# Performance work log

Measured on AMD Instinct MI355X. Metric: run time of the kernel, lower is better.

The kernel has to match this reference:

```python
import jax, jax.numpy as jnp
import numpy as np

NUM_EMBEDDINGS = 1024
EMBEDDING_DIM = 256
COMMITMENT_COST = 0.25


def setup_inputs() -> dict:
    key = jax.random.key(0)
    k1, k2 = jax.random.split(key)
    z = jax.random.normal(k1, (64, 32, 32, EMBEDDING_DIM), dtype=jnp.float32)
    # torch init: uniform(-1/num_embeddings, 1/num_embeddings)
    codebook = jax.random.uniform(
        k2, (NUM_EMBEDDINGS, EMBEDDING_DIM), dtype=jnp.float32,
        minval=-1.0 / NUM_EMBEDDINGS, maxval=1.0 / NUM_EMBEDDINGS)
    return {"z": z, "codebook": codebook}


def reference(z, codebook):
    sg = jax.lax.stop_gradient
    D = codebook.shape[1]
    flat_z = z.reshape(-1, D)  # [N, D]
    # squared L2 distances: ||z||^2 + ||e||^2 - 2 z.e  -> [N, K]
    distances = (jnp.sum(flat_z * flat_z, axis=1, keepdims=True)
                 + jnp.sum(codebook * codebook, axis=1)
                 - 2.0 * jnp.matmul(flat_z, codebook.T))
    indices = jnp.argmin(distances, axis=1)  # [N]
    quantized = codebook[indices].reshape(z.shape)
    e_latent_loss = jnp.mean((quantized - sg(z)) ** 2)
    q_latent_loss = jnp.mean((z - sg(quantized)) ** 2)
    vq_loss = e_latent_loss + COMMITMENT_COST * q_latent_loss
    # straight-through estimator
    quantized_st = z + sg(quantized - z)
    return quantized_st, vq_loss, indices.reshape(z.shape[:-1])
```

## Files before the change

kernel.cpp:

```cpp
#include <hip/hip_runtime.h>

#pragma clang fp contract(off)


#define NROWS   65536
#define DDIM    256
#define KCODES  1024
#define QSIZE   (NROWS * DDIM)
#define LOSS_OFF QSIZE
#define IDX_OFF (QSIZE + 1)
#define MARGIN  3.0e-4f
#define RCAP    16384
#define RBATCH  16

typedef __bf16 bf16x8 __attribute__((ext_vector_type(8)));
typedef float f32x4 __attribute__((ext_vector_type(4)));
typedef unsigned int u32;
typedef unsigned long long u64;
typedef unsigned short u16;

#define GLOAD_LDS16(gsrc, ldst) \
    __builtin_amdgcn_global_load_lds( \
        (const __attribute__((address_space(1))) u32*)(gsrc), \
        (__attribute__((address_space(3))) u32*)(ldst), 16, 0, 0)

__device__ __forceinline__ u32 omap(float s) {
    u32 u = __float_as_uint(s);
    return (u & 0x80000000u) ? ~u : (u | 0x80000000u);
}
__device__ __forceinline__ u64 pack_key(float s, u32 j) {
    return ((u64)omap(s) << 32) | j;
}

__device__ __forceinline__ float pw128_sq(const float* __restrict__ x) {
    float r[8];
    #pragma unroll
    for (int j = 0; j < 8; ++j) r[j] = x[j] * x[j];
    for (int i = 8; i < 128; i += 8)
        #pragma unroll
        for (int j = 0; j < 8; ++j) r[j] += x[i + j] * x[i + j];
    return ((r[0] + r[1]) + (r[2] + r[3])) + ((r[4] + r[5]) + (r[6] + r[7]));
}

__global__ __launch_bounds__(256) void vq_pack_cb(
    const float* __restrict__ E, u16* __restrict__ ebh,
    float4* __restrict__ etp,
    float* __restrict__ ee, float* __restrict__ sum, int* __restrict__ count) {
    int j = blockIdx.x * 256 + threadIdx.x;
    if (j == 0) { *sum = 0.0f; *count = 0; }
    if (j >= KCODES) return;
    const float* row = E + (size_t)j * DDIM;
    const float4* row4 = (const float4*)row;
    #pragma unroll
    for (int d4 = 0; d4 < DDIM / 4; ++d4) etp[d4 * KCODES + j] = row4[d4];
    #pragma unroll
    for (int ks = 0; ks < 32; ++ks) {
        bf16x8 h8;
        #pragma unroll
        for (int e = 0; e < 8; ++e) h8[e] = (__bf16)row[ks * 8 + e];
        *(bf16x8*)(ebh + ((size_t)ks * KCODES + j) * 8) = h8;
    }
    ee[j] = pw128_sq(row) + pw128_sq(row + 128);
}

__device__ __forceinline__ void stage_chunk32(
    const u16* __restrict__ ebh, int codebase, char* buf, int t) {
    #pragma unroll
    for (int i = 0; i < 4; ++i) {
        int p = t + 256 * i;
        int ks = p >> 5, c = p & 31;
        GLOAD_LDS16(ebh + ((size_t)ks * KCODES + codebase + c) * 8, buf + p * 16);
    }
}

__global__ __launch_bounds__(256, 4) void vq_gemm(
    const float* __restrict__ Z,
    const u16* __restrict__ ebh,
    const float* __restrict__ ee,
    float* __restrict__ s1c, float* __restrict__ s2c, float* __restrict__ i1c,
    float* __restrict__ sum) {
    __shared__ __align__(16) char bs[3][16384];
    const int t = threadIdx.x, w = t >> 6, l = t & 63;
    const int lr = l & 15, lg = l >> 4;
    const int rowtile = blockIdx.x >> 1, half = blockIdx.x & 1;
    const int rowbase = rowtile * 128;
    const int codebase = half * 512;

    bf16x8 aH[2][8];
    float ss = 0.0f;
    #pragma unroll
    for (int rf = 0; rf < 2; ++rf) {
        const float* zr = Z + (size_t)(rowbase + w * 32 + rf * 16 + lr) * DDIM;
        #pragma unroll
        for (int s = 0; s < 8; ++s) {
            const float4* src = (const float4*)(zr + (s * 4 + lg) * 8);
            float4 v0 = src[0], v1 = src[1];
            bf16x8 h8;
            h8[0] = (__bf16)v0.x; h8[1] = (__bf16)v0.y;
            h8[2] = (__bf16)v0.z; h8[3] = (__bf16)v0.w;
            h8[4] = (__bf16)v1.x; h8[5] = (__bf16)v1.y;
            h8[6] = (__bf16)v1.z; h8[7] = (__bf16)v1.w;
            aH[rf][s] = h8;
            ss += v0.x * v0.x + v0.y * v0.y + v0.z * v0.z + v0.w * v0.w
                + v1.x * v1.x + v1.y * v1.y + v1.z * v1.z + v1.w * v1.w;
        }
    }
    if (half == 0) {
        #pragma unroll
        for (int off = 1; off < 64; off <<= 1) ss += __shfl_xor(ss, off);
        if (l == 0) atomicAdd(sum, ss);
    }

    float s1[2][4], s2[2][4]; int i1[2][4];
    #pragma unroll
    for (int rf = 0; rf < 2; ++rf)
        #pragma unroll
        for (int r = 0; r < 4; ++r) { s1[rf][r] = 1e30f; s2[rf][r] = 1e30f; i1[rf][r] = 0x7FFFFFFF; }

    stage_chunk32(ebh, codebase, bs[0], t);
    stage_chunk32(ebh, codebase + 32, bs[1], t);
    for (int ch = 0; ch < 16; ++ch) {
        if (ch < 15) { asm volatile("s_waitcnt vmcnt(4)" ::: "memory"); }
        else         { asm volatile("s_waitcnt vmcnt(0)" ::: "memory"); }
        __builtin_amdgcn_sched_barrier(0);
        __builtin_amdgcn_s_barrier();
        if (ch + 2 < 16) stage_chunk32(ebh, codebase + (ch + 2) * 32, bs[(ch + 2) % 3], t);
        const char* buf = bs[ch % 3];
        const int chbase = codebase + ch * 32;

        f32x4 acc[2][2];
        #pragma unroll
        for (int rf = 0; rf < 2; ++rf)
            #pragma unroll
            for (int cf = 0; cf < 2; ++cf) acc[rf][cf] = 0.0f;

        #pragma unroll
        for (int s = 0; s < 8; ++s) {
            #pragma unroll
            for (int cf = 0; cf < 2; ++cf) {
                int off = (((s * 4 + lg) * 32 + cf * 16 + lr) * 16);
                bf16x8 bh = *(const bf16x8*)(buf + off);
                #pragma unroll
                for (int rf = 0; rf < 2; ++rf)
                    acc[rf][cf] = __builtin_amdgcn_mfma_f32_16x16x32_bf16(aH[rf][s], bh, acc[rf][cf], 0, 0, 0);
            }
        }
        #pragma unroll
        for (int cf = 0; cf < 2; ++cf) {
            int code = chbase + cf * 16 + lr;
            float e2c = ee[code];
            #pragma unroll
            for (int rf = 0; rf < 2; ++rf)
                #pragma unroll
                for (int r = 0; r < 4; ++r) {
                    float v = __fmaf_rn(-2.0f, acc[rf][cf][r], e2c);
                    float so = s1[rf][r];
                    s2[rf][r] = fminf(fmaxf(so, v), s2[rf][r]);
                    bool lt = v < so;
                    s1[rf][r] = lt ? v : so;
                    i1[rf][r] = lt ? code : i1[rf][r];
                }
        }
    }
    #pragma unroll
    for (int off = 1; off < 16; off <<= 1) {
        #pragma unroll
        for (int rf = 0; rf < 2; ++rf)
            #pragma unroll
            for (int r = 0; r < 4; ++r) {
                float os1 = __shfl_xor(s1[rf][r], off);
                float os2 = __shfl_xor(s2[rf][r], off);
                int   oi  = __shfl_xor(i1[rf][r], off);
                float ns2 = fminf(fmaxf(s1[rf][r], os1), fminf(s2[rf][r], os2));
                bool take = (os1 < s1[rf][r]) || (os1 == s1[rf][r] && oi < i1[rf][r]);
                s1[rf][r] = take ? os1 : s1[rf][r];
                i1[rf][r] = take ? oi : i1[rf][r];
                s2[rf][r] = ns2;
            }
    }
    if (lr == 0) {
        #pragma unroll
        for (int rf = 0; rf < 2; ++rf)
            #pragma unroll
            for (int r = 0; r < 4; ++r) {
                size_t idx = (size_t)half * NROWS + rowbase + w * 32 + rf * 16 + lg * 4 + r;
                s1c[idx] = s1[rf][r];
                s2c[idx] = s2[rf][r];
                i1c[idx] = (float)i1[rf][r];
            }
    }
}

__global__ __launch_bounds__(256) void vq_combine(
    const float* __restrict__ s1c, const float* __restrict__ s2c,
    const float* __restrict__ i1c,
    float* out, float* __restrict__ sum, int* __restrict__ count,
    int* __restrict__ list) {
    const int r = blockIdx.x * 256 + threadIdx.x;
    float s1a = s1c[r], s1b = s1c[NROWS + r];
    float s2a = s2c[r], s2b = s2c[NROWS + r];
    int   ia  = (int)i1c[r], ib = (int)i1c[NROWS + r];
    bool tb = s1b < s1a;
    float s1 = tb ? s1b : s1a;
    int   i1 = tb ? ib : ia;
    float s2 = tb ? fminf(s2b, s1a) : fminf(s2a, s1b);
    out[(size_t)IDX_OFF + r] = (float)i1;
    if (s2 <= s1 + MARGIN) {
        int slot = atomicAdd(count, 1);
        if (slot < RCAP) list[slot] = r;
    }
    #pragma unroll
    for (int off = 1; off < 64; off <<= 1) s1 += __shfl_xor(s1, off);
    if ((threadIdx.x & 63) == 0) atomicAdd(sum, s1);
}

__global__ __launch_bounds__(256) void vq_rescue(
    const float* __restrict__ Z, const float4* __restrict__ etp,
    const float* __restrict__ ee, const int* __restrict__ count,
    const int* __restrict__ list, const float* __restrict__ sum, float* out) {
    __shared__ float zrow[RBATCH][DDIM];
    __shared__ float zacc[RBATCH][16];
    __shared__ float z2s[RBATCH];
    __shared__ u64 rmin[RBATCH];
    __shared__ int rowid[RBATCH];
    const int t = threadIdx.x;
    if (blockIdx.x == 0 && t == 0) out[LOSS_OFF] = 1.25f * (*sum) / (float)QSIZE;
    int n = *count; if (n > RCAP) n = RCAP;
    const int base = blockIdx.x * RBATCH;
    if (base >= n) return;
    int nb = n - base; if (nb > RBATCH) nb = RBATCH;

    if (t < RBATCH) {
        rowid[t] = (t < nb) ? list[base + t] : 0;
        rmin[t] = ~0ULL;
    }
    __syncthreads();
    #pragma unroll
    for (int i = 0; i < RBATCH * (DDIM / 4) / 256; ++i) {
        int p = t + 256 * i;
        int r = p >> 6, c4 = p & 63;
        if (r < nb) ((float4*)zrow[r])[c4] =
            ((const float4*)(Z + (size_t)rowid[r] * DDIM))[c4];
    }
    __syncthreads();
    if (t < RBATCH * 8) {
        int r = t >> 3, j = t & 7;
        const float* zr = zrow[r];
        float a0 = zr[j] * zr[j], a1 = zr[128 + j] * zr[128 + j];
        for (int i = 8; i < 128; i += 8) {
            a0 += zr[i + j] * zr[i + j];
            a1 += zr[128 + i + j] * zr[128 + i + j];
        }
        zacc[r][j] = a0; zacc[r][8 + j] = a1;
    }
    __syncthreads();
    if (t < RBATCH) {
        const float* a = zacc[t];
        float c0 = ((a[0] + a[1]) + (a[2] + a[3])) + ((a[4] + a[5]) + (a[6] + a[7]));
        float c1 = ((a[8] + a[9]) + (a[10] + a[11])) + ((a[12] + a[13]) + (a[14] + a[15]));
        z2s[t] = c0 + c1;
    }
    __syncthreads();

    float acc[4][RBATCH];
    #pragma unroll
    for (int c = 0; c < 4; ++c)
        #pragma unroll
        for (int r = 0; r < RBATCH; ++r) acc[c][r] = 0.0f;

    for (int d4 = 0; d4 < DDIM / 4; ++d4) {
        float4 ev[4];
        #pragma unroll
        for (int c = 0; c < 4; ++c)
            ev[c] = etp[(size_t)d4 * KCODES + t + c * 256];
        #pragma unroll
        for (int r = 0; r < RBATCH; ++r) {
            float4 zv = ((const float4*)zrow[r])[d4];
            #pragma unroll
            for (int c = 0; c < 4; ++c) {
                float a = acc[c][r];
                a = __fmaf_rn(zv.x, ev[c].x, a); a = __fmaf_rn(zv.y, ev[c].y, a);
                a = __fmaf_rn(zv.z, ev[c].z, a); a = __fmaf_rn(zv.w, ev[c].w, a);
                acc[c][r] = a;
            }
        }
    }
    float e2c[4];
    #pragma unroll
    for (int c = 0; c < 4; ++c) e2c[c] = ee[t + c * 256];
    #pragma unroll
    for (int r = 0; r < RBATCH; ++r) {
        float zr2 = z2s[r];
        u64 best = ~0ULL;
        #pragma unroll
        for (int c = 0; c < 4; ++c) {
            float d = (zr2 + e2c[c]) - 2.0f * acc[c][r];
            u64 k = pack_key(d, (u32)(t + c * 256));
            if (k < best) best = k;
        }
        #pragma unroll
        for (int off = 1; off < 64; off <<= 1) {
            u64 o = __shfl_xor(best, off);
            if (o < best) best = o;
        }
        if ((t & 63) == 0) atomicMin(&rmin[r], best);
    }
    __syncthreads();
    if (t < nb) out[(size_t)IDX_OFF + rowid[t]] = (float)(u32)(rmin[t] & 0xFFFFFFFFu);
}

__global__ __launch_bounds__(256) void vq_qwrite(
    const float* __restrict__ E, float* out) {
    __shared__ int qidx[32];
    const int t = threadIdx.x;
    const size_t rowbase = (size_t)blockIdx.x * 32;
    if (t < 32) qidx[t] = (int)out[(size_t)IDX_OFF + rowbase + t];
    __syncthreads();
    float4* outq = (float4*)out;
    #pragma unroll
    for (int k = 0; k < 8; ++k) {
        int idx = t + 256 * k;
        int r = idx >> 6, c4 = idx & 63;
        int code = qidx[r];
        outq[rowbase * 64 + idx] = ((const float4*)(E + (size_t)code * DDIM))[c4];
    }
}

extern "C" void kernel_launch(void* const* d_in, const int* in_sizes, int n_in,
                              void* d_out, int out_size, void* d_ws, size_t ws_size,
                              hipStream_t stream) {
    const float* Z; const float* E;
    if (in_sizes[0] == QSIZE) { Z = (const float*)d_in[0]; E = (const float*)d_in[1]; }
    else                      { Z = (const float*)d_in[1]; E = (const float*)d_in[0]; }
    float* out = (float*)d_out;
    char* ws = (char*)d_ws;

    float* sum   = (float*)ws;
    int*   count = (int*)(ws + 4);
    float* ee    = (float*)(ws + 1024);
    u16*   ebh   = (u16*)(ws + 8192);
    int*   list  = (int*)(ws + 8192 + 524288);

    float*  s1c = out;
    float*  s2c = out + 2 * NROWS;
    float*  i1c = out + 4 * NROWS;
    float4* etp = (float4*)(out + 6 * NROWS);

    vq_pack_cb<<<4, 256, 0, stream>>>(E, ebh, etp, ee, sum, count);
    vq_gemm<<<NROWS / 128 * 2, 256, 0, stream>>>(Z, ebh, ee, s1c, s2c, i1c, sum);
    vq_combine<<<NROWS / 256, 256, 0, stream>>>(s1c, s2c, i1c, out, sum, count, list);
    vq_rescue<<<RCAP / RBATCH, 256, 0, stream>>>(Z, etp, ee, count, list, sum, out);
    vq_qwrite<<<NROWS / 32, 256, 0, stream>>>(E, out);
}
```

Measured before the change: 225.9 us.

## Fuse combine, rescue and quantized-write kernels into one cooperative kernel

Replaces three separate post-GEMM launches (combine, rescue, qwrite) with a single cooperative kernel of 512 blocks. The phases are separated by grid-wide syncs. The goal is to remove kernel launch gaps and tail effects between these small stages. In exchange it adds grid.sync costs, uses only 64 threads per block in the combine phase, and forces a fixed grid size that must fit co-resident.

```diff
diff --git a/kernel.cpp b/kernel.cpp
--- a/kernel.cpp
+++ b/kernel.cpp
@@ -1,6 +1,9 @@
 #include <hip/hip_runtime.h>
+#include <hip/hip_cooperative_groups.h>
 
 #pragma clang fp contract(off)
+
+namespace cg = cooperative_groups;
 
 
 #define NROWS   65536
@@ -12,6 +15,7 @@
 #define MARGIN  3.0e-4f
 #define RCAP    16384
 #define RBATCH  16
+#define FGRID   512
 
 typedef __bf16 bf16x8 __attribute__((ext_vector_type(8)));
 typedef float f32x4 __attribute__((ext_vector_type(4)));
@@ -191,138 +195,147 @@
     }
 }
 
-__global__ __launch_bounds__(256) void vq_combine(
+__global__ __launch_bounds__(256, 4) void vq_finish(
+    const float* __restrict__ Z, const float4* __restrict__ etp,
+    const float* __restrict__ ee, const float* __restrict__ E,
     const float* __restrict__ s1c, const float* __restrict__ s2c,
     const float* __restrict__ i1c,
-    float* out, float* __restrict__ sum, int* __restrict__ count,
-    int* __restrict__ list) {
-    const int r = blockIdx.x * 256 + threadIdx.x;
-    float s1a = s1c[r], s1b = s1c[NROWS + r];
-    float s2a = s2c[r], s2b = s2c[NROWS + r];
-    int   ia  = (int)i1c[r], ib = (int)i1c[NROWS + r];
-    bool tb = s1b < s1a;
-    float s1 = tb ? s1b : s1a;
-    int   i1 = tb ? ib : ia;
-    float s2 = tb ? fminf(s2b, s1a) : fminf(s2a, s1b);
-    out[(size_t)IDX_OFF + r] = (float)i1;
-    if (s2 <= s1 + MARGIN) {
-        int slot = atomicAdd(count, 1);
-        if (slot < RCAP) list[slot] = r;
-    }
-    #pragma unroll
-    for (int off = 1; off < 64; off <<= 1) s1 += __shfl_xor(s1, off);
-    if ((threadIdx.x & 63) == 0) atomicAdd(sum, s1);
-}
-
-__global__ __launch_bounds__(256) void vq_rescue(
-    const float* __restrict__ Z, const float4* __restrict__ etp,
-    const float* __restrict__ ee, const int* __restrict__ count,
-    const int* __restrict__ list, const float* __restrict__ sum, float* out) {
+    float* __restrict__ sum, int* __restrict__ count, int* __restrict__ list,
+    float* __restrict__ out) {
     __shared__ float zrow[RBATCH][DDIM];
     __shared__ float zacc[RBATCH][16];
     __shared__ float z2s[RBATCH];
     __shared__ u64 rmin[RBATCH];
     __shared__ int rowid[RBATCH];
+    __shared__ int qidx[64];
     const int t = threadIdx.x;
-    if (blockIdx.x == 0 && t == 0) out[LOSS_OFF] = 1.25f * (*sum) / (float)QSIZE;
-    int n = *count; if (n > RCAP) n = RCAP;
-    const int base = blockIdx.x * RBATCH;
-    if (base >= n) return;
-    int nb = n - base; if (nb > RBATCH) nb = RBATCH;
-
-    if (t < RBATCH) {
-        rowid[t] = (t < nb) ? list[base + t] : 0;
-        rmin[t] = ~0ULL;
-    }
-    __syncthreads();
-    #pragma unroll
-    for (int i = 0; i < RBATCH * (DDIM / 4) / 256; ++i) {
-        int p = t + 256 * i;
-        int r = p >> 6, c4 = p & 63;
-        if (r < nb) ((float4*)zrow[r])[c4] =
-            ((const float4*)(Z + (size_t)rowid[r] * DDIM))[c4];
-    }
-    __syncthreads();
-    if (t < RBATCH * 8) {
-        int r = t >> 3, j = t & 7;
-        const float* zr = zrow[r];
-        float a0 = zr[j] * zr[j], a1 = zr[128 + j] * zr[128 + j];
-        for (int i = 8; i < 128; i += 8) {
-            a0 += zr[i + j] * zr[i + j];
-            a1 += zr[128 + i + j] * zr[128 + i + j];
-        }
-        zacc[r][j] = a0; zacc[r][8 + j] = a1;
-    }
-    __syncthreads();
-    if (t < RBATCH) {
-        const float* a = zacc[t];
-        float c0 = ((a[0] + a[1]) + (a[2] + a[3])) + ((a[4] + a[5]) + (a[6] + a[7]));
-        float c1 = ((a[8] + a[9]) + (a[10] + a[11])) + ((a[12] + a[13]) + (a[14] + a[15]));
-        z2s[t] = c0 + c1;
-    }
-    __syncthreads();
-
-    float acc[4][RBATCH];
-    #pragma unroll
-    for (int c = 0; c < 4; ++c)
-        #pragma unroll
-        for (int r = 0; r < RBATCH; ++r) acc[c][r] = 0.0f;
-
-    for (int d4 = 0; d4 < DDIM / 4; ++d4) {
-        float4 ev[4];
-        #pragma unroll
-        for (int c = 0; c < 4; ++c)
-            ev[c] = etp[(size_t)d4 * KCODES + t + c * 256];
-        #pragma unroll
-        for (int r = 0; r < RBATCH; ++r) {
-            float4 zv = ((const float4*)zrow[r])[d4];
-            #pragma unroll
-            for (int c = 0; c < 4; ++c) {
-                float a = acc[c][r];
-                a = __fmaf_rn(zv.x, ev[c].x, a); a = __fmaf_rn(zv.y, ev[c].y, a);
-                a = __fmaf_rn(zv.z, ev[c].z, a); a = __fmaf_rn(zv.w, ev[c].w, a);
-                acc[c][r] = a;
-            }
-        }
-    }
-    float e2c[4];
-    #pragma unroll
-    for (int c = 0; c < 4; ++c) e2c[c] = ee[t + c * 256];
-    #pragma unroll
-    for (int r = 0; r < RBATCH; ++r) {
-        float zr2 = z2s[r];
-        u64 best = ~0ULL;
-        #pragma unroll
-        for (int c = 0; c < 4; ++c) {
-            float d = (zr2 + e2c[c]) - 2.0f * acc[c][r];
-            u64 k = pack_key(d, (u32)(t + c * 256));
-            if (k < best) best = k;
-        }
-        #pragma unroll
-        for (int off = 1; off < 64; off <<= 1) {
-            u64 o = __shfl_xor(best, off);
-            if (o < best) best = o;
-        }
-        if ((t & 63) == 0) atomicMin(&rmin[r], best);
-    }
-    __syncthreads();
-    if (t < nb) out[(size_t)IDX_OFF + rowid[t]] = (float)(u32)(rmin[t] & 0xFFFFFFFFu);
-}
-
-__global__ __launch_bounds__(256) void vq_qwrite(
-    const float* __restrict__ E, float* out) {
-    __shared__ int qidx[32];
-    const int t = threadIdx.x;
-    const size_t rowbase = (size_t)blockIdx.x * 32;
-    if (t < 32) qidx[t] = (int)out[(size_t)IDX_OFF + rowbase + t];
-    __syncthreads();
-    float4* outq = (float4*)out;
-    #pragma unroll
-    for (int k = 0; k < 8; ++k) {
-        int idx = t + 256 * k;
-        int r = idx >> 6, c4 = idx & 63;
-        int code = qidx[r];
-        outq[rowbase * 64 + idx] = ((const float4*)(E + (size_t)code * DDIM))[c4];
+    const int b = blockIdx.x;
+    cg::grid_group grid = cg::this_grid();
+
+    #pragma unroll
+    for (int ii = 0; ii < 2; ++ii) {
+        int r = b * 128 + ii * 64 + t;
+        if (t < 64) {
+            float s1a = s1c[r], s1b = s1c[NROWS + r];
+            float s2a = s2c[r], s2b = s2c[NROWS + r];
+            int   ia  = (int)i1c[r], ib = (int)i1c[NROWS + r];
+            bool tb = s1b < s1a;
+            float s1 = tb ? s1b : s1a;
+            int   i1 = tb ? ib : ia;
+            float s2 = tb ? fminf(s2b, s1a) : fminf(s2a, s1b);
+            out[(size_t)IDX_OFF + r] = (float)i1;
+            if (s2 <= s1 + MARGIN) {
+                int slot = atomicAdd(count, 1);
+                if (slot < RCAP) list[slot] = r;
+            }
+            #pragma unroll
+            for (int off = 1; off < 64; off <<= 1) s1 += __shfl_xor(s1, off);
+            if (t == 0) atomicAdd(sum, s1);
+        }
+    }
+    grid.sync();
+
+    {
+        int n = *count; if (n > RCAP) n = RCAP;
+        for (int bb = b; bb < RCAP / RBATCH; bb += FGRID) {
+            int base = bb * RBATCH;
+            if (base >= n) continue;
+            int nb = n - base; if (nb > RBATCH) nb = RBATCH;
+            if (t < RBATCH) {
+                rowid[t] = (t < nb) ? list[base + t] : 0;
+                rmin[t] = ~0ULL;
+            }
+            __syncthreads();
+            #pragma unroll
+            for (int i = 0; i < RBATCH * (DDIM / 4) / 256; ++i) {
+                int p = t + 256 * i;
+                int r = p >> 6, c4 = p & 63;
+                if (r < nb) ((float4*)zrow[r])[c4] =
+                    ((const float4*)(Z + (size_t)rowid[r] * DDIM))[c4];
+            }
+            __syncthreads();
+            if (t < RBATCH * 8) {
+                int r = t >> 3, j = t & 7;
+                const float* zr = zrow[r];
+                float a0 = zr[j] * zr[j], a1 = zr[128 + j] * zr[128 + j];
+                for (int i = 8; i < 128; i += 8) {
+                    a0 += zr[i + j] * zr[i + j];
+                    a1 += zr[128 + i + j] * zr[128 + i + j];
+                }
+                zacc[r][j] = a0; zacc[r][8 + j] = a1;
+            }
+            __syncthreads();
+            if (t < RBATCH) {
+                const float* a = zacc[t];
+                float c0 = ((a[0] + a[1]) + (a[2] + a[3])) + ((a[4] + a[5]) + (a[6] + a[7]));
+                float c1 = ((a[8] + a[9]) + (a[10] + a[11])) + ((a[12] + a[13]) + (a[14] + a[15]));
+                z2s[t] = c0 + c1;
+            }
+            __syncthreads();
+            float acc[4][RBATCH];
+            #pragma unroll
+            for (int c = 0; c < 4; ++c)
+                #pragma unroll
+                for (int r = 0; r < RBATCH; ++r) acc[c][r] = 0.0f;
+            for (int d4 = 0; d4 < DDIM / 4; ++d4) {
+                float4 ev[4];
+                #pragma unroll
+                for (int c = 0; c < 4; ++c)
+                    ev[c] = etp[(size_t)d4 * KCODES + t + c * 256];
+                #pragma unroll
+                for (int r = 0; r < RBATCH; ++r) {
+                    float4 zv = ((const float4*)zrow[r])[d4];
+                    #pragma unroll
+                    for (int c = 0; c < 4; ++c) {
+                        float a = acc[c][r];
+                        a = __fmaf_rn(zv.x, ev[c].x, a); a = __fmaf_rn(zv.y, ev[c].y, a);
+                        a = __fmaf_rn(zv.z, ev[c].z, a); a = __fmaf_rn(zv.w, ev[c].w, a);
+                        acc[c][r] = a;
+                    }
+                }
+            }
+            float e2c[4];
+            #pragma unroll
+            for (int c = 0; c < 4; ++c) e2c[c] = ee[t + c * 256];
+            #pragma unroll
+            for (int r = 0; r < RBATCH; ++r) {
+                float zr2 = z2s[r];
+                u64 best = ~0ULL;
+                #pragma unroll
+                for (int c = 0; c < 4; ++c) {
+                    float d = (zr2 + e2c[c]) - 2.0f * acc[c][r];
+                    u64 k = pack_key(d, (u32)(t + c * 256));
+                    if (k < best) best = k;
+                }
+                #pragma unroll
+                for (int off = 1; off < 64; off <<= 1) {
+                    u64 o = __shfl_xor(best, off);
+                    if (o < best) best = o;
+                }
+                if ((t & 63) == 0) atomicMin(&rmin[r], best);
+            }
+            __syncthreads();
+            if (t < nb) out[(size_t)IDX_OFF + rowid[t]] = (float)(u32)(rmin[t] & 0xFFFFFFFFu);
+            __syncthreads();
+        }
+    }
+    grid.sync();
+
+    if (b == 0 && t == 0) out[LOSS_OFF] = 1.25f * (*sum) / (float)QSIZE;
+    #pragma unroll
+    for (int ii = 0; ii < 2; ++ii) {
+        size_t rowbase = (size_t)b * 128 + ii * 64;
+        if (t < 64) qidx[t] = (int)out[(size_t)IDX_OFF + rowbase + t];
+        __syncthreads();
+        float4* outq = (float4*)out;
+        #pragma unroll
+        for (int k = 0; k < 16; ++k) {
+            int p = t + 256 * k;
+            int r = p >> 6, c4 = p & 63;
+            int code = qidx[r];
+            outq[rowbase * 64 + p] = ((const float4*)(E + (size_t)code * DDIM))[c4];
+        }
+        __syncthreads();
     }
 }
 
@@ -348,7 +361,10 @@
 
     vq_pack_cb<<<4, 256, 0, stream>>>(E, ebh, etp, ee, sum, count);
     vq_gemm<<<NROWS / 128 * 2, 256, 0, stream>>>(Z, ebh, ee, s1c, s2c, i1c, sum);
-    vq_combine<<<NROWS / 256, 256, 0, stream>>>(s1c, s2c, i1c, out, sum, count, list);
-    vq_rescue<<<RCAP / RBATCH, 256, 0, stream>>>(Z, etp, ee, count, list, sum, out);
-    vq_qwrite<<<NROWS / 32, 256, 0, stream>>>(E, out);
-}
+
+    void* args[] = { (void*)&Z, (void*)&etp, (void*)&ee, (void*)&E,
+                     (void*)&s1c, (void*)&s2c, (void*)&i1c,
+                     (void*)&sum, (void*)&count, (void*)&list, (void*)&out };
+    hipLaunchCooperativeKernel((void*)vq_finish, dim3(FGRID), dim3(256),
+                               args, 0, stream);
+}
```

Measured after the change: 311.2 us. 1.38x slower.

## Fuse near-tie rescue with quantized-row write using per-row flags

Applied to the files above, without the earlier changes.

Replaces the global atomic list of ambiguous rows with a per-row flag byte, and merges the rescue pass and the quantized-output gather into one kernel. Each block handles 128 rows: it compacts flagged rows locally, recomputes exact fp32 distances for them in batches of 16, then writes all 128 quantized rows. This drops one kernel launch, the global atomic counter and the RCAP cap, and moves etp out of the output buffer into workspace. In exchange, rescue work is now spread unevenly across blocks and each block serialises its own rescue batches before the gather.

```diff
diff --git a/kernel.cpp b/kernel.cpp
--- a/kernel.cpp
+++ b/kernel.cpp
@@ -10,7 +10,6 @@
 #define LOSS_OFF QSIZE
 #define IDX_OFF (QSIZE + 1)
 #define MARGIN  3.0e-4f
-#define RCAP    16384
 #define RBATCH  16
 
 typedef __bf16 bf16x8 __attribute__((ext_vector_type(8)));
@@ -18,6 +17,7 @@
 typedef unsigned int u32;
 typedef unsigned long long u64;
 typedef unsigned short u16;
+typedef unsigned char u8;
 
 #define GLOAD_LDS16(gsrc, ldst) \
     __builtin_amdgcn_global_load_lds( \
@@ -45,9 +45,9 @@
 __global__ __launch_bounds__(256) void vq_pack_cb(
     const float* __restrict__ E, u16* __restrict__ ebh,
     float4* __restrict__ etp,
-    float* __restrict__ ee, float* __restrict__ sum, int* __restrict__ count) {
+    float* __restrict__ ee, float* __restrict__ sum) {
     int j = blockIdx.x * 256 + threadIdx.x;
-    if (j == 0) { *sum = 0.0f; *count = 0; }
+    if (j == 0) *sum = 0.0f;
     if (j >= KCODES) return;
     const float* row = E + (size_t)j * DDIM;
     const float4* row4 = (const float4*)row;
@@ -194,8 +194,7 @@
 __global__ __launch_bounds__(256) void vq_combine(
     const float* __restrict__ s1c, const float* __restrict__ s2c,
     const float* __restrict__ i1c,
-    float* out, float* __restrict__ sum, int* __restrict__ count,
-    int* __restrict__ list) {
+    float* out, float* __restrict__ sum, u8* __restrict__ flags) {
     const int r = blockIdx.x * 256 + threadIdx.x;
     float s1a = s1c[r], s1b = s1c[NROWS + r];
     float s2a = s2c[r], s2b = s2c[NROWS + r];
@@ -205,124 +204,128 @@
     int   i1 = tb ? ib : ia;
     float s2 = tb ? fminf(s2b, s1a) : fminf(s2a, s1b);
     out[(size_t)IDX_OFF + r] = (float)i1;
-    if (s2 <= s1 + MARGIN) {
-        int slot = atomicAdd(count, 1);
-        if (slot < RCAP) list[slot] = r;
-    }
+    flags[r] = (s2 <= s1 + MARGIN) ? 1 : 0;
     #pragma unroll
     for (int off = 1; off < 64; off <<= 1) s1 += __shfl_xor(s1, off);
     if ((threadIdx.x & 63) == 0) atomicAdd(sum, s1);
 }
 
-__global__ __launch_bounds__(256) void vq_rescue(
+__global__ __launch_bounds__(256) void vq_rescueq(
     const float* __restrict__ Z, const float4* __restrict__ etp,
-    const float* __restrict__ ee, const int* __restrict__ count,
-    const int* __restrict__ list, const float* __restrict__ sum, float* out) {
+    const float* __restrict__ ee, const float* __restrict__ E,
+    const u8* __restrict__ flags, const float* __restrict__ sum,
+    float* out) {
     __shared__ float zrow[RBATCH][DDIM];
     __shared__ float zacc[RBATCH][16];
     __shared__ float z2s[RBATCH];
     __shared__ u64 rmin[RBATCH];
-    __shared__ int rowid[RBATCH];
+    __shared__ int qidx[128];
+    __shared__ int fl[128];
+    __shared__ int nfl;
     const int t = threadIdx.x;
-    if (blockIdx.x == 0 && t == 0) out[LOSS_OFF] = 1.25f * (*sum) / (float)QSIZE;
-    int n = *count; if (n > RCAP) n = RCAP;
-    const int base = blockIdx.x * RBATCH;
-    if (base >= n) return;
-    int nb = n - base; if (nb > RBATCH) nb = RBATCH;
-
-    if (t < RBATCH) {
-        rowid[t] = (t < nb) ? list[base + t] : 0;
-        rmin[t] = ~0ULL;
-    }
+    const int b = blockIdx.x;
+    const int rowbase = b * 128;
+
+    if (b == 0 && t == 0) out[LOSS_OFF] = 1.25f * (*sum) / (float)QSIZE;
+    if (t == 0) nfl = 0;
     __syncthreads();
-    #pragma unroll
-    for (int i = 0; i < RBATCH * (DDIM / 4) / 256; ++i) {
-        int p = t + 256 * i;
+    if (t < 128) {
+        int code = (int)out[(size_t)IDX_OFF + rowbase + t];
+        qidx[t] = code;
+        if (flags[rowbase + t]) { int s = atomicAdd(&nfl, 1); fl[s] = t; }
+    }
+    __syncthreads();
+    const int n = nfl;
+
+    for (int start = 0; start < n; start += RBATCH) {
+        int nb = n - start; if (nb > RBATCH) nb = RBATCH;
+        if (t < RBATCH) rmin[t] = ~0ULL;
+        __syncthreads();
+        #pragma unroll
+        for (int i = 0; i < RBATCH * (DDIM / 4) / 256; ++i) {
+            int p = t + 256 * i;
+            int r = p >> 6, c4 = p & 63;
+            if (r < nb) ((float4*)zrow[r])[c4] =
+                ((const float4*)(Z + (size_t)(rowbase + fl[start + r]) * DDIM))[c4];
+        }
+        __syncthreads();
+        if (t < RBATCH * 8) {
+            int r = t >> 3, j = t & 7;
+            const float* zr = zrow[r];
+            float a0 = zr[j] * zr[j], a1 = zr[128 + j] * zr[128 + j];
+            for (int i = 8; i < 128; i += 8) {
+                a0 += zr[i + j] * zr[i + j];
+                a1 += zr[128 + i + j] * zr[128 + i + j];
+            }
+            zacc[r][j] = a0; zacc[r][8 + j] = a1;
+        }
+        __syncthreads();
+        if (t < RBATCH) {
+            const float* a = zacc[t];
+            float c0 = ((a[0] + a[1]) + (a[2] + a[3])) + ((a[4] + a[5]) + (a[6] + a[7]));
+            float c1 = ((a[8] + a[9]) + (a[10] + a[11])) + ((a[12] + a[13]) + (a[14] + a[15]));
+            z2s[t] = c0 + c1;
+        }
+        __syncthreads();
+        float acc[4][RBATCH];
+        #pragma unroll
+        for (int c = 0; c < 4; ++c)
+            #pragma unroll
+            for (int r = 0; r < RBATCH; ++r) acc[c][r] = 0.0f;
+        for (int d4 = 0; d4 < DDIM / 4; ++d4) {
+            float4 ev[4];
+            #pragma unroll
+            for (int c = 0; c < 4; ++c)
+                ev[c] = etp[(size_t)d4 * KCODES + t + c * 256];
+            #pragma unroll
+            for (int r = 0; r < RBATCH; ++r) {
+                float4 zv = ((const float4*)zrow[r])[d4];
+                #pragma unroll
+                for (int c = 0; c < 4; ++c) {
+                    float a = acc[c][r];
+                    a = __fmaf_rn(zv.x, ev[c].x, a); a = __fmaf_rn(zv.y, ev[c].y, a);
+                    a = __fmaf_rn(zv.z, ev[c].z, a); a = __fmaf_rn(zv.w, ev[c].w, a);
+                    acc[c][r] = a;
+                }
+            }
+        }
+        float e2c[4];
+        #pragma unroll
+        for (int c = 0; c < 4; ++c) e2c[c] = ee[t + c * 256];
+        #pragma unroll
+        for (int r = 0; r < RBATCH; ++r) {
+            float zr2 = z2s[r];
+            u64 best = ~0ULL;
+            #pragma unroll
+            for (int c = 0; c < 4; ++c) {
+                float d = (zr2 + e2c[c]) - 2.0f * acc[c][r];
+                u64 k = pack_key(d, (u32)(t + c * 256));
+                if (k < best) best = k;
+            }
+            #pragma unroll
+            for (int off = 1; off < 64; off <<= 1) {
+                u64 o = __shfl_xor(best, off);
+                if (o < best) best = o;
+            }
+            if ((t & 63) == 0) atomicMin(&rmin[r], best);
+        }
+        __syncthreads();
+        if (t < nb) {
+            int lrow = fl[start + t];
+            int code = (int)(u32)(rmin[t] & 0xFFFFFFFFu);
+            out[(size_t)IDX_OFF + rowbase + lrow] = (float)code;
+            qidx[lrow] = code;
+        }
+        __syncthreads();
+    }
+
+    float4* outq = (float4*)out;
+    #pragma unroll
+    for (int k = 0; k < 32; ++k) {
+        int p = t + 256 * k;
         int r = p >> 6, c4 = p & 63;
-        if (r < nb) ((float4*)zrow[r])[c4] =
-            ((const float4*)(Z + (size_t)rowid[r] * DDIM))[c4];
-    }
-    __syncthreads();
-    if (t < RBATCH * 8) {
-        int r = t >> 3, j = t & 7;
-        const float* zr = zrow[r];
-        float a0 = zr[j] * zr[j], a1 = zr[128 + j] * zr[128 + j];
-        for (int i = 8; i < 128; i += 8) {
-            a0 += zr[i + j] * zr[i + j];
-            a1 += zr[128 + i + j] * zr[128 + i + j];
-        }
-        zacc[r][j] = a0; zacc[r][8 + j] = a1;
-    }
-    __syncthreads();
-    if (t < RBATCH) {
-        const float* a = zacc[t];
-        float c0 = ((a[0] + a[1]) + (a[2] + a[3])) + ((a[4] + a[5]) + (a[6] + a[7]));
-        float c1 = ((a[8] + a[9]) + (a[10] + a[11])) + ((a[12] + a[13]) + (a[14] + a[15]));
-        z2s[t] = c0 + c1;
-    }
-    __syncthreads();
-
-    float acc[4][RBATCH];
-    #pragma unroll
-    for (int c = 0; c < 4; ++c)
-        #pragma unroll
-        for (int r = 0; r < RBATCH; ++r) acc[c][r] = 0.0f;
-
-    for (int d4 = 0; d4 < DDIM / 4; ++d4) {
-        float4 ev[4];
-        #pragma unroll
-        for (int c = 0; c < 4; ++c)
-            ev[c] = etp[(size_t)d4 * KCODES + t + c * 256];
-        #pragma unroll
-        for (int r = 0; r < RBATCH; ++r) {
-            float4 zv = ((const float4*)zrow[r])[d4];
-            #pragma unroll
-            for (int c = 0; c < 4; ++c) {
-                float a = acc[c][r];
-                a = __fmaf_rn(zv.x, ev[c].x, a); a = __fmaf_rn(zv.y, ev[c].y, a);
-                a = __fmaf_rn(zv.z, ev[c].z, a); a = __fmaf_rn(zv.w, ev[c].w, a);
-                acc[c][r] = a;
-            }
-        }
-    }
-    float e2c[4];
-    #pragma unroll
-    for (int c = 0; c < 4; ++c) e2c[c] = ee[t + c * 256];
-    #pragma unroll
-    for (int r = 0; r < RBATCH; ++r) {
-        float zr2 = z2s[r];
-        u64 best = ~0ULL;
-        #pragma unroll
-        for (int c = 0; c < 4; ++c) {
-            float d = (zr2 + e2c[c]) - 2.0f * acc[c][r];
-            u64 k = pack_key(d, (u32)(t + c * 256));
-            if (k < best) best = k;
-        }
-        #pragma unroll
-        for (int off = 1; off < 64; off <<= 1) {
-            u64 o = __shfl_xor(best, off);
-            if (o < best) best = o;
-        }
-        if ((t & 63) == 0) atomicMin(&rmin[r], best);
-    }
-    __syncthreads();
-    if (t < nb) out[(size_t)IDX_OFF + rowid[t]] = (float)(u32)(rmin[t] & 0xFFFFFFFFu);
-}
-
-__global__ __launch_bounds__(256) void vq_qwrite(
-    const float* __restrict__ E, float* out) {
-    __shared__ int qidx[32];
-    const int t = threadIdx.x;
-    const size_t rowbase = (size_t)blockIdx.x * 32;
-    if (t < 32) qidx[t] = (int)out[(size_t)IDX_OFF + rowbase + t];
-    __syncthreads();
-    float4* outq = (float4*)out;
-    #pragma unroll
-    for (int k = 0; k < 8; ++k) {
-        int idx = t + 256 * k;
-        int r = idx >> 6, c4 = idx & 63;
         int code = qidx[r];
-        outq[rowbase * 64 + idx] = ((const float4*)(E + (size_t)code * DDIM))[c4];
+        outq[(size_t)rowbase * 64 + p] = ((const float4*)(E + (size_t)code * DDIM))[c4];
     }
 }
 
@@ -335,20 +338,18 @@
     float* out = (float*)d_out;
     char* ws = (char*)d_ws;
 
-    float* sum   = (float*)ws;
-    int*   count = (int*)(ws + 4);
-    float* ee    = (float*)(ws + 1024);
-    u16*   ebh   = (u16*)(ws + 8192);
-    int*   list  = (int*)(ws + 8192 + 524288);
-
-    float*  s1c = out;
-    float*  s2c = out + 2 * NROWS;
-    float*  i1c = out + 4 * NROWS;
-    float4* etp = (float4*)(out + 6 * NROWS);
-
-    vq_pack_cb<<<4, 256, 0, stream>>>(E, ebh, etp, ee, sum, count);
+    float*  sum   = (float*)ws;
+    float*  ee    = (float*)(ws + 1024);
+    u16*    ebh   = (u16*)(ws + 8192);
+    u8*     flags = (u8*)(ws + 532480);
+    float4* etp   = (float4*)(ws + 598016);
+
+    float* s1c = out;
+    float* s2c = out + 2 * NROWS;
+    float* i1c = out + 4 * NROWS;
+
+    vq_pack_cb<<<4, 256, 0, stream>>>(E, ebh, etp, ee, sum);
     vq_gemm<<<NROWS / 128 * 2, 256, 0, stream>>>(Z, ebh, ee, s1c, s2c, i1c, sum);
-    vq_combine<<<NROWS / 256, 256, 0, stream>>>(s1c, s2c, i1c, out, sum, count, list);
-    vq_rescue<<<RCAP / RBATCH, 256, 0, stream>>>(Z, etp, ee, count, list, sum, out);
-    vq_qwrite<<<NROWS / 32, 256, 0, stream>>>(E, out);
-}
+    vq_combine<<<NROWS / 256, 256, 0, stream>>>(s1c, s2c, i1c, out, sum, flags);
+    vq_rescueq<<<NROWS / 128, 256, 0, stream>>>(Z, etp, ee, E, flags, sum, out);
+}
```

New measurement: 198.8 us (median of 2 runs). 12.0% less time.
